# Optimization experiments

Hardware: AMD Instinct MI355X
Metric: run time of the kernel (lower is better)

## Reference

```python
import jax, jax.numpy as jnp
import numpy as np

B, S, D, H = 2, 1024, 1024, 16
DH = D // H            # dim per head = 64
MAX_REL = 32           # max relative positions
ROPE_BASE = 10000.0


def entmax15(X, axis=-1):
    """1.5-entmax with full sort (k=None path of the torch code)."""
    X = (X - jnp.max(X, axis=axis, keepdims=True)) / 2.0
    Xsrt = -jnp.sort(-X, axis=axis)                       # descending sort
    d = X.shape[axis]
    rho = jnp.arange(1, d + 1, dtype=X.dtype)             # broadcasts on last axis
    mean = jnp.cumsum(Xsrt, axis=axis) / rho
    mean_sq = jnp.cumsum(Xsrt * Xsrt, axis=axis) / rho
    ss = rho * (mean_sq - mean * mean)
    delta = (1.0 - ss) / rho
    tau = mean - jnp.sqrt(jnp.clip(delta, 0.0))
    support = jnp.sum(tau <= Xsrt, axis=axis, keepdims=True)
    tau_star = jnp.take_along_axis(tau, support - 1, axis=axis)
    Y = jnp.clip(X - tau_star, 0.0)
    return Y * Y


def _rope(x, cos, sin):
    # x: [B,S,H,DH]; cos/sin: [S, DH//2]; complex mult on (even,odd) pairs
    xe, xo = x[..., 0::2], x[..., 1::2]
    c = cos[None, :, None, :]
    s = sin[None, :, None, :]
    re = xe * c - xo * s
    im = xe * s + xo * c
    return jnp.stack([re, im], axis=-1).reshape(x.shape)


def setup_inputs() -> dict:
    key = jax.random.key(0)
    ks = jax.random.split(key, 10)
    sc = 0.02
    x = jax.random.normal(ks[0], (B, S, D), dtype=jnp.float32)
    w_q = jax.random.normal(ks[1], (D, D), dtype=jnp.float32) * sc
    w_k = jax.random.normal(ks[2], (D, D), dtype=jnp.float32) * sc
    w_v = jax.random.normal(ks[3], (D, D), dtype=jnp.float32) * sc
    w_o = jax.random.normal(ks[4], (D, D), dtype=jnp.float32) * sc
    b_q = jnp.zeros((D,), jnp.float32)
    b_k = jnp.zeros((D,), jnp.float32)
    b_v = jnp.zeros((D,), jnp.float32)
    b_o = jnp.zeros((D,), jnp.float32)
    rel_emb = jax.random.normal(ks[5], (2 * MAX_REL + 1, DH), dtype=jnp.float32) * sc
    inv_freq = 1.0 / (ROPE_BASE ** (np.arange(0, DH, 2, dtype=np.float32) / DH))
    ang = np.arange(S, dtype=np.float32)[:, None] * inv_freq[None, :]
    rope_cos = jnp.asarray(np.cos(ang), jnp.float32)
    rope_sin = jnp.asarray(np.sin(ang), jnp.float32)
    return {"x": x, "w_q": w_q, "b_q": b_q, "w_k": w_k, "b_k": b_k,
            "w_v": w_v, "b_v": b_v, "w_o": w_o, "b_o": b_o,
            "rel_emb": rel_emb, "rope_cos": rope_cos, "rope_sin": rope_sin}


def reference(x, w_q, b_q, w_k, b_k, w_v, b_v, w_o, b_o, rel_emb, rope_cos, rope_sin):
    # QKV projections -> [B,S,H,DH]
    q = (x @ w_q + b_q).reshape(B, S, H, DH)
    k = (x @ w_k + b_k).reshape(B, S, H, DH)
    v = (x @ w_v + b_v).reshape(B, S, H, DH).transpose(0, 2, 1, 3)  # [B,H,S,DH]
    # RoPE on q, k (applied in [B,S,H,DH] layout like the torch code)
    q = _rope(q, rope_cos, rope_sin).transpose(0, 2, 1, 3)  # [B,H,S,DH]
    k = _rope(k, rope_cos, rope_sin).transpose(0, 2, 1, 3)
    q = q / jnp.sqrt(jnp.asarray(DH, q.dtype))
    # content scores
    scores = jnp.einsum('bhqd,bhkd->bhqk', q, k)
    # relative position bias (Shaw et al.), shared embedding for keys & values
    r = jnp.arange(S)
    dist = jnp.clip(r[None, :] - r[:, None], -MAX_REL, MAX_REL) + MAX_REL  # [S,S]
    rel = rel_emb[dist]                                                   # [S,S,DH]
    scores = scores + jnp.einsum('bhqd,qkd->bhqk', q, rel)
    # sparse normalization
    attn = entmax15(scores, axis=-1)
    # context + relative-position values
    ctx = jnp.einsum('bhqk,bhkd->bhqd', attn, v) + jnp.einsum('bhqk,qkd->bhqd', attn, rel)
    out = ctx.transpose(0, 2, 1, 3).reshape(B, S, D) @ w_o + b_o
    return out
```

## Files before the change

kernel.cpp:

```cpp
#include <hip/hip_runtime.h>

typedef __attribute__((ext_vector_type(8))) short s8v;
typedef __attribute__((ext_vector_type(4))) short s4v;
typedef __attribute__((ext_vector_type(4))) float f4v;

__device__ __forceinline__ short f2bf(float f){
  union { float f; unsigned u; } v; v.f = f;
  unsigned r = v.u + 0x7fffu + ((v.u >> 16) & 1u);
  return (short)(r >> 16);
}
__device__ __forceinline__ float bf2f(short s){
  union { unsigned u; float f; } v; v.u = ((unsigned)(unsigned short)s) << 16; return v.f;
}

__global__ __launch_bounds__(256) void prep_k(const float* __restrict__ w_q, const float* __restrict__ w_k,
                                              const float* __restrict__ w_v, const float* __restrict__ w_o,
                                              const float* __restrict__ x, const float* __restrict__ rel,
                                              short* __restrict__ wqkvT, short* __restrict__ woT,
                                              short* __restrict__ xb, short* __restrict__ relb,
                                              short* __restrict__ relT){
  int z = blockIdx.z;
  if (z < 4){
    __shared__ float t[64][65];
    const float* in = (z==0) ? w_q : (z==1) ? w_k : (z==2) ? w_v : w_o;
    short* out = (z==3) ? woT : (wqkvT + ((size_t)z<<20));
    int c0 = blockIdx.x*64, r0 = blockIdx.y*64;
    int tx = threadIdx.x & 63, ty = threadIdx.x >> 6;
    #pragma unroll
    for (int i=0;i<16;i++){ int r = ty + i*4; t[r][tx] = in[(size_t)(r0+r)*1024 + c0+tx]; }
    __syncthreads();
    #pragma unroll
    for (int i=0;i<16;i++){ int cc = ty + i*4; out[(size_t)(c0+cc)*1024 + r0+tx] = f2bf(t[tx][cc]); }
    if (z==3 && blockIdx.x==0 && blockIdx.y==0){
      for (int e = threadIdx.x; e < 65*64; e += 256){
        int j = e >> 6, d = e & 63;
        short bv = f2bf(rel[e]);
        relb[e] = bv;
        relT[d*72 + j] = bv;
      }
    }
  } else {
    int bid = (z-4)*256 + blockIdx.y*16 + blockIdx.x;
    int i = bid*256 + threadIdx.x;
    #pragma unroll
    for (int p=0;p<4;p++){
      int idx = p*131072 + i;
      f4v v = ((const f4v*)x)[idx];
      s4v o; o[0]=f2bf(v[0]); o[1]=f2bf(v[1]); o[2]=f2bf(v[2]); o[3]=f2bf(v[3]);
      ((s4v*)xb)[idx] = o;
    }
  }
}

__device__ __forceinline__ void gemm128_core(const short* __restrict__ A, const short* __restrict__ Bt,
                                             int m0, int n0, short* As, short* Bs, f4v acc[4][4]){
  int tid = threadIdx.x;
  int lane = tid & 63, wave = tid >> 6;
  int wr = wave >> 1, wc = wave & 1, g = lane >> 4, c = lane & 15;
  int srow = tid >> 3, su = tid & 7;
  for (int k0 = 0; k0 < 1024; k0 += 64){
    #pragma unroll
    for (int p=0;p<4;p++){
      int r = srow + p*32;
      int u = su ^ (r & 7);
      *(s8v*)(&As[r*64 + u*8]) = *(const s8v*)(A + (size_t)(m0+r)*1024 + k0 + su*8);
      *(s8v*)(&Bs[r*64 + u*8]) = *(const s8v*)(Bt + (size_t)(n0+r)*1024 + k0 + su*8);
    }
    __syncthreads();
    #pragma unroll
    for (int ks=0;ks<2;ks++){
      s8v a[4], b[4];
      int pu = ((ks*4 + g) ^ (c & 7))*8;
      #pragma unroll
      for (int mi=0;mi<4;mi++) a[mi] = *(const s8v*)(&As[(wr*64 + mi*16 + c)*64 + pu]);
      #pragma unroll
      for (int ni=0;ni<4;ni++) b[ni] = *(const s8v*)(&Bs[(wc*64 + ni*16 + c)*64 + pu]);
      #pragma unroll
      for (int mi=0;mi<4;mi++)
        #pragma unroll
        for (int ni=0;ni<4;ni++)
          acc[mi][ni] = __builtin_amdgcn_mfma_f32_16x16x32_bf16(a[mi], b[ni], acc[mi][ni], 0,0,0);
    }
    __syncthreads();
  }
}

__global__ __launch_bounds__(256) void gemm_qkv_k(const short* __restrict__ A, const short* __restrict__ Bt,
                                                  const float* __restrict__ b_q, const float* __restrict__ b_k,
                                                  const float* __restrict__ b_v,
                                                  const float* __restrict__ cs, const float* __restrict__ sn,
                                                  short* __restrict__ Qb, short* __restrict__ Kb,
                                                  short* __restrict__ Vt){
  __shared__ __align__(16) char lbuf[33792];
  short* As = (short*)lbuf;
  short* Bs = (short*)(lbuf + 16384);
  short* st = (short*)lbuf;
  int flat = blockIdx.x;
  int swz = (flat & 7)*48 + (flat >> 3);
  int m0 = (swz / 24) * 128, n0 = (swz % 24) * 128;
  int lane = threadIdx.x & 63, wave = threadIdx.x >> 6;
  int wr = wave >> 1, wc = wave & 1, g = lane >> 4, c = lane & 15;
  f4v acc[4][4] = {};
  gemm128_core(A, Bt, m0, n0, As, Bs, acc);

  int sec = n0 >> 10;
  const float* bias = (sec==0) ? b_q : (sec==1) ? b_k : b_v;
  int b = m0 >> 10, s0 = m0 & 1023, hbase = (n0 & 1023) >> 6;
  #pragma unroll
  for (int mi=0;mi<4;mi++)
    #pragma unroll
    for (int ni=0;ni<4;ni++){
      int cl = wc*64 + ni*16 + c;
      int hcol = (n0 & 1023) + cl;
      float bi = bias[hcol];
      int d = hcol & 63, ifr = d >> 1;
      #pragma unroll
      for (int i=0;i<4;i++){
        int rl = wr*64 + mi*16 + g*4 + i;
        float v = acc[mi][ni][i] + bi;
        if (sec < 2){
          int s = s0 + rl;
          float co = cs[s*32 + ifr], si = sn[s*32 + ifr];
          float p = __shfl_xor(v, 1, 64);
          float o = (cl & 1) ? fmaf(p, si, v*co) : fmaf(v, co, -(p*si));
          if (sec == 0) o *= 0.125f;
          v = o;
        }
        st[rl*132 + cl] = f2bf(v);
      }
    }
  __syncthreads();
  if (sec < 2){
    short* dst = (sec==0) ? Qb : Kb;
    for (int e = threadIdx.x; e < 128*32; e += 256){
      int row = e >> 5, cl4 = (e & 31)*4;
      int h = hbase + (cl4 >> 6), d = cl4 & 63;
      s4v o = *(const s4v*)(&st[row*132 + cl4]);
      *(s4v*)(&dst[((size_t)(b*16+h)*1024 + s0 + row)*64 + d]) = o;
    }
  } else {
    for (int e = threadIdx.x; e < 128*32; e += 256){
      int cl = e >> 5, s4 = (e & 31)*4;
      int h = hbase + (cl >> 6), dl = cl & 63;
      s4v o;
      o[0] = st[(s4+0)*132 + cl]; o[1] = st[(s4+1)*132 + cl];
      o[2] = st[(s4+2)*132 + cl]; o[3] = st[(s4+3)*132 + cl];
      *(s4v*)(&Vt[(size_t)(b*16+h)*65536 + (size_t)dl*1024 + s0 + s4]) = o;
    }
  }
}

__global__ __launch_bounds__(256) void gemm_out_k(const short* __restrict__ A, const short* __restrict__ Bt,
                                                  const float* __restrict__ bias, float* __restrict__ C){
  __shared__ __align__(16) short As[128*64];
  __shared__ __align__(16) short Bs[128*64];
  int flat = blockIdx.x;
  int swz = (flat & 7)*16 + (flat >> 3);
  int n0 = (swz & 7)*128, m0 = (swz >> 3)*128;
  int lane = threadIdx.x & 63, wave = threadIdx.x >> 6;
  int wr = wave >> 1, wc = wave & 1, g = lane >> 4, c = lane & 15;
  f4v acc[4][4] = {};
  gemm128_core(A, Bt, m0, n0, As, Bs, acc);
  #pragma unroll
  for (int mi=0;mi<4;mi++)
    #pragma unroll
    for (int ni=0;ni<4;ni++){
      int col = n0 + wc*64 + ni*16 + c;
      float bi = bias[col];
      #pragma unroll
      for (int i=0;i<4;i++){
        int row = m0 + wr*64 + mi*16 + g*4 + i;
        C[(size_t)row*1024 + col] = acc[mi][ni][i] + bi;
      }
    }
}

#define ATPAD 1028
__global__ __launch_bounds__(256,4) void attn_fused_k(const short* __restrict__ Qb, const short* __restrict__ Kb,
                                                      const short* __restrict__ relb, const short* __restrict__ relT,
                                                      const short* __restrict__ Vt, short* __restrict__ ctxb){
  __shared__ __align__(16) short pb_b[16][66];
  __shared__ __align__(16) float wrow[16][68];
  __shared__ __align__(16) short attn_l[16][ATPAD];
  float2* red = (float2*)&pb_b[0][0];

  int lane = threadIdx.x & 63, wave = threadIdx.x >> 6;
  int g = lane >> 4, c = lane & 15;
  int flat = blockIdx.x;
  int swz = (flat & 7)*256 + (flat >> 3);
  int bh = swz >> 6, q0 = (swz & 63)*16;
  const short* Qh = Qb + (size_t)bh*65536;
  const short* Kh = Kb + (size_t)bh*65536;
  const short* Vh = Vt + (size_t)bh*65536;

  for (int e = threadIdx.x; e < 16*68; e += 256) ((float*)wrow)[e] = 0.f;

  s8v qa0 = *(const s8v*)(Qh + (q0+c)*64 + g*8);
  s8v qa1 = *(const s8v*)(Qh + (q0+c)*64 + 32 + g*8);

  {
    int ntile = (wave==3) ? 2 : 1;
    for (int t=0; t<ntile; t++){
      int jt = (t==0) ? wave : 4;
      int j = jt*16 + c;
      s8v rb0 = {}, rb1 = {};
      if (j < 65){
        rb0 = *(const s8v*)(relb + j*64 + g*8);
        rb1 = *(const s8v*)(relb + j*64 + 32 + g*8);
      }
      f4v pa = {};
      pa = __builtin_amdgcn_mfma_f32_16x16x32_bf16(qa0, rb0, pa, 0,0,0);
      pa = __builtin_amdgcn_mfma_f32_16x16x32_bf16(qa1, rb1, pa, 0,0,0);
      if (j < 65){
        #pragma unroll
        for (int i=0;i<4;i++) pb_b[g*4+i][j] = f2bf(pa[i]);
      }
    }
  }
  __syncthreads();

  int q = q0 + c;
  int kc0 = wave*256;
  f4v x[16];
  #pragma unroll
  for (int t=0;t<16;t++){
    f4v ini;
    #pragma unroll
    for (int i=0;i<4;i++){
      int k = kc0 + t*16 + g*4 + i;
      int jj = min(max(k - q, -32), 32) + 32;
      ini[i] = bf2f(pb_b[c][jj]);
    }
    const short* kp = Kh + (kc0 + t*16 + c)*64 + g*8;
    s8v ka0 = *(const s8v*)(kp);
    s8v ka1 = *(const s8v*)(kp + 32);
    ini = __builtin_amdgcn_mfma_f32_16x16x32_bf16(ka0, qa0, ini, 0,0,0);
    x[t] = __builtin_amdgcn_mfma_f32_16x16x32_bf16(ka1, qa1, ini, 0,0,0);
  }
  __syncthreads();

  float m0v = -1e30f, m1v = -1e30f, m2v = -1e30f, m3v = -1e30f;
  #pragma unroll
  for (int t=0;t<16;t++){
    m0v = fmaxf(m0v, x[t][0]); m1v = fmaxf(m1v, x[t][1]);
    m2v = fmaxf(m2v, x[t][2]); m3v = fmaxf(m3v, x[t][3]);
  }
  float mx = fmaxf(fmaxf(m0v,m1v), fmaxf(m2v,m3v));
  mx = fmaxf(mx, __shfl_xor(mx, 16, 64));
  mx = fmaxf(mx, __shfl_xor(mx, 32, 64));
  if (g == 0) red[wave*16 + c] = make_float2(mx, 0.f);
  __syncthreads();
  {
    float2 r0 = red[c], r1 = red[16+c], r2 = red[32+c], r3 = red[48+c];
    mx = fmaxf(fmaxf(r0.x, r1.x), fmaxf(r2.x, r3.x));
  }

  float theta = mx - 2.0f;
  for (int it=0; it<7; it++){
    float s1a=0.f,s1b=0.f,s1c=0.f,s1d=0.f, s2a=0.f,s2b=0.f,s2c=0.f,s2d=0.f;
    #pragma unroll
    for (int t=0;t<16;t++){
      float t0 = fmaxf(x[t][0]-theta, 0.f); s1a += t0; s2a = fmaf(t0,t0,s2a);
      float t1 = fmaxf(x[t][1]-theta, 0.f); s1b += t1; s2b = fmaf(t1,t1,s2b);
      float t2 = fmaxf(x[t][2]-theta, 0.f); s1c += t2; s2c = fmaf(t2,t2,s2c);
      float t3 = fmaxf(x[t][3]-theta, 0.f); s1d += t3; s2d = fmaf(t3,t3,s2d);
    }
    float S1 = (s1a+s1b)+(s1c+s1d), S2 = (s2a+s2b)+(s2c+s2d);
    S1 += __shfl_xor(S1, 16, 64); S2 += __shfl_xor(S2, 16, 64);
    S1 += __shfl_xor(S1, 32, 64); S2 += __shfl_xor(S2, 32, 64);
    int pp = (it+1)&1;
    if (g == 0) red[(pp*4 + wave)*16 + c] = make_float2(S1, S2);
    __syncthreads();
    float2 r0 = red[pp*64 + c], r1 = red[pp*64 + 16+c], r2 = red[pp*64 + 32+c], r3 = red[pp*64 + 48+c];
    S1 = (r0.x+r1.x)+(r2.x+r3.x);
    S2 = (r0.y+r1.y)+(r2.y+r3.y);
    theta += (S2 - 4.0f)/(2.0f*S1);
  }

  float w0p = 0.f, w64p = 0.f;
  #pragma unroll
  for (int t=0;t<16;t++){
    s4v pk;
    #pragma unroll
    for (int i=0;i<4;i++){
      int k = kc0 + t*16 + g*4 + i;
      float tt = fmaxf(x[t][i]-theta, 0.f)*0.5f;
      float a = tt*tt;
      pk[i] = f2bf(a);
      int raw = k - q;
      if (raw <= -32) w0p += a;
      else if (raw >= 32) w64p += a;
      else wrow[c][raw+32] = a;
    }
    *(s4v*)(&attn_l[c][kc0 + t*16 + g*4]) = pk;
  }
  w0p += __shfl_xor(w0p, 16, 64); w64p += __shfl_xor(w64p, 16, 64);
  w0p += __shfl_xor(w0p, 32, 64); w64p += __shfl_xor(w64p, 32, 64);
  if (g == 0) red[wave*16 + c] = make_float2(w0p, w64p);
  __syncthreads();
  if (wave == 0 && g == 0){
    float2 r0 = red[c], r1 = red[16+c], r2 = red[32+c], r3 = red[48+c];
    wrow[c][0]  = (r0.x+r1.x)+(r2.x+r3.x);
    wrow[c][64] = (r0.y+r1.y)+(r2.y+r3.y);
  }
  __syncthreads();

  f4v acc = {};
  #pragma unroll 8
  for (int kk=0; kk<32; kk++){
    s8v af = *(const s8v*)(&attn_l[c][kk*32 + g*8]);
    s8v bf = *(const s8v*)(Vh + (size_t)(wave*16+c)*1024 + kk*32 + g*8);
    acc = __builtin_amdgcn_mfma_f32_16x16x32_bf16(af, bf, acc, 0,0,0);
  }
  {
    const float* wp = &wrow[c][0];
    f4v a_ = *(const f4v*)(wp + g*8);
    f4v b_ = *(const f4v*)(wp + g*8 + 4);
    f4v c_ = *(const f4v*)(wp + 32 + g*8);
    f4v d_ = *(const f4v*)(wp + 32 + g*8 + 4);
    s8v wa0, wa1;
    wa0[0]=f2bf(a_[0]); wa0[1]=f2bf(a_[1]); wa0[2]=f2bf(a_[2]); wa0[3]=f2bf(a_[3]);
    wa0[4]=f2bf(b_[0]); wa0[5]=f2bf(b_[1]); wa0[6]=f2bf(b_[2]); wa0[7]=f2bf(b_[3]);
    wa1[0]=f2bf(c_[0]); wa1[1]=f2bf(c_[1]); wa1[2]=f2bf(c_[2]); wa1[3]=f2bf(c_[3]);
    wa1[4]=f2bf(d_[0]); wa1[5]=f2bf(d_[1]); wa1[6]=f2bf(d_[2]); wa1[7]=f2bf(d_[3]);
    s8v rb0 = *(const s8v*)(relT + (wave*16+c)*72 + g*8);
    s8v rb1 = *(const s8v*)(relT + (wave*16+c)*72 + 32 + g*8);
    acc = __builtin_amdgcn_mfma_f32_16x16x32_bf16(wa0, rb0, acc, 0,0,0);
    acc = __builtin_amdgcn_mfma_f32_16x16x32_bf16(wa1, rb1, acc, 0,0,0);
  }
  int b = bh >> 4, h = bh & 15, d = wave*16 + c;
  float rl64 = bf2f(relT[d*72 + 64]);
  #pragma unroll
  for (int i=0;i<4;i++){
    int r = g*4+i;
    float s = acc[i] + wrow[r][64]*rl64;
    ctxb[((size_t)(b*1024 + q0 + r))*1024 + h*64 + d] = f2bf(s);
  }
}

extern "C" void kernel_launch(void* const* d_in, const int* in_sizes, int n_in,
                              void* d_out, int out_size, void* d_ws, size_t ws_size,
                              hipStream_t stream) {
  (void)in_sizes; (void)n_in; (void)out_size; (void)ws_size;
  const float* x    = (const float*)d_in[0];
  const float* w_q  = (const float*)d_in[1];
  const float* b_q  = (const float*)d_in[2];
  const float* w_k  = (const float*)d_in[3];
  const float* b_k  = (const float*)d_in[4];
  const float* w_v  = (const float*)d_in[5];
  const float* b_v  = (const float*)d_in[6];
  const float* w_o  = (const float*)d_in[7];
  const float* b_o  = (const float*)d_in[8];
  const float* rel  = (const float*)d_in[9];
  const float* rcos = (const float*)d_in[10];
  const float* rsin = (const float*)d_in[11];
  float* out = (float*)d_out;

  char* w = (char*)d_ws;
  short* xb    = (short*)(w);
  short* wqkvT = (short*)(w + ((size_t)4<<20));
  short* woT   = (short*)(w + ((size_t)10<<20));
  short* Qb    = (short*)(w + ((size_t)12<<20));
  short* Kb    = (short*)(w + ((size_t)16<<20));
  short* Vt    = (short*)(w + ((size_t)20<<20));
  short* ctxb  = (short*)(w + ((size_t)24<<20));
  short* relb  = (short*)(w + ((size_t)28<<20));
  short* relT  = (short*)(w + ((size_t)28<<20) + 65536);

  prep_k<<<dim3(16,16,6), 256, 0, stream>>>(w_q, w_k, w_v, w_o, x, rel, wqkvT, woT, xb, relb, relT);
  gemm_qkv_k<<<384, 256, 0, stream>>>(xb, wqkvT, b_q, b_k, b_v, rcos, rsin, Qb, Kb, Vt);
  attn_fused_k<<<2048, 256, 0, stream>>>(Qb, Kb, relb, relT, Vt, ctxb);
  gemm_out_k<<<128, 256, 0, stream>>>(ctxb, woT, b_o, out);
}
```

Measured before the change: 138.4 us.

## Use direct global-to-LDS loads in GEMM and streamline entmax attention epilogue

The GEMM core now stages A and B tiles with global_load_lds 16-byte direct loads instead of register round-trips, and drops the XOR swizzle on the LDS layout. The attention kernel skips per-element relative-bias gathers and per-element bucket logic for tiles that lie entirely outside the relative window. It also vectorises the entmax threshold loops, uses hardware packed bf16 conversion, and raises wave priority around the PV MFMA loop. Removing the swizzle may bring back LDS bank conflicts on the fragment reads.

```diff
diff --git a/kernel.cpp b/kernel.cpp
--- a/kernel.cpp
+++ b/kernel.cpp
@@ -11,6 +11,10 @@
 }
 __device__ __forceinline__ float bf2f(short s){
   union { unsigned u; float f; } v; v.u = ((unsigned)(unsigned short)s) << 16; return v.f;
+}
+__device__ __forceinline__ void gload16(const void* g, void* l){
+  __builtin_amdgcn_global_load_lds((const __attribute__((address_space(1))) unsigned int*)g,
+                                   (__attribute__((address_space(3))) unsigned int*)l, 16, 0, 0);
 }
 
 __global__ __launch_bounds__(256) void prep_k(const float* __restrict__ w_q, const float* __restrict__ w_k,
@@ -57,20 +61,20 @@
   int tid = threadIdx.x;
   int lane = tid & 63, wave = tid >> 6;
   int wr = wave >> 1, wc = wave & 1, g = lane >> 4, c = lane & 15;
-  int srow = tid >> 3, su = tid & 7;
+  int lrow = lane >> 3, lcol = (lane & 7)*8;
   for (int k0 = 0; k0 < 1024; k0 += 64){
     #pragma unroll
     for (int p=0;p<4;p++){
-      int r = srow + p*32;
-      int u = su ^ (r & 7);
-      *(s8v*)(&As[r*64 + u*8]) = *(const s8v*)(A + (size_t)(m0+r)*1024 + k0 + su*8);
-      *(s8v*)(&Bs[r*64 + u*8]) = *(const s8v*)(Bt + (size_t)(n0+r)*1024 + k0 + su*8);
+      int r0 = wave*32 + p*8;
+      int row = r0 + lrow;
+      gload16(A  + (size_t)(m0+row)*1024 + k0 + lcol, &As[r0*64]);
+      gload16(Bt + (size_t)(n0+row)*1024 + k0 + lcol, &Bs[r0*64]);
     }
     __syncthreads();
     #pragma unroll
     for (int ks=0;ks<2;ks++){
       s8v a[4], b[4];
-      int pu = ((ks*4 + g) ^ (c & 7))*8;
+      int pu = ks*32 + g*8;
       #pragma unroll
       for (int mi=0;mi<4;mi++) a[mi] = *(const s8v*)(&As[(wr*64 + mi*16 + c)*64 + pu]);
       #pragma unroll
@@ -221,15 +225,23 @@
 
   int q = q0 + c;
   int kc0 = wave*256;
+  int Lb = q0 - 32 - kc0;
+  int Ub = q0 + 47 - kc0;
+  float pb0  = bf2f(pb_b[c][0]);
+  float pb64 = bf2f(pb_b[c][64]);
   f4v x[16];
   #pragma unroll
   for (int t=0;t<16;t++){
     f4v ini;
-    #pragma unroll
-    for (int i=0;i<4;i++){
-      int k = kc0 + t*16 + g*4 + i;
-      int jj = min(max(k - q, -32), 32) + 32;
-      ini[i] = bf2f(pb_b[c][jj]);
+    if (t*16+15 <= Lb){ ini[0]=pb0; ini[1]=pb0; ini[2]=pb0; ini[3]=pb0; }
+    else if (t*16 >= Ub){ ini[0]=pb64; ini[1]=pb64; ini[2]=pb64; ini[3]=pb64; }
+    else {
+      #pragma unroll
+      for (int i=0;i<4;i++){
+        int k = kc0 + t*16 + g*4 + i;
+        int jj = min(max(k - q, -32), 32) + 32;
+        ini[i] = bf2f(pb_b[c][jj]);
+      }
     }
     const short* kp = Kh + (kc0 + t*16 + c)*64 + g*8;
     s8v ka0 = *(const s8v*)(kp);
@@ -239,13 +251,13 @@
   }
   __syncthreads();
 
-  float m0v = -1e30f, m1v = -1e30f, m2v = -1e30f, m3v = -1e30f;
+  f4v m4 = x[0];
   #pragma unroll
-  for (int t=0;t<16;t++){
-    m0v = fmaxf(m0v, x[t][0]); m1v = fmaxf(m1v, x[t][1]);
-    m2v = fmaxf(m2v, x[t][2]); m3v = fmaxf(m3v, x[t][3]);
-  }
-  float mx = fmaxf(fmaxf(m0v,m1v), fmaxf(m2v,m3v));
+  for (int t=1;t<16;t++){
+    m4[0]=fmaxf(m4[0],x[t][0]); m4[1]=fmaxf(m4[1],x[t][1]);
+    m4[2]=fmaxf(m4[2],x[t][2]); m4[3]=fmaxf(m4[3],x[t][3]);
+  }
+  float mx = fmaxf(fmaxf(m4[0],m4[1]), fmaxf(m4[2],m4[3]));
   mx = fmaxf(mx, __shfl_xor(mx, 16, 64));
   mx = fmaxf(mx, __shfl_xor(mx, 32, 64));
   if (g == 0) red[wave*16 + c] = make_float2(mx, 0.f);
@@ -257,15 +269,18 @@
 
   float theta = mx - 2.0f;
   for (int it=0; it<7; it++){
-    float s1a=0.f,s1b=0.f,s1c=0.f,s1d=0.f, s2a=0.f,s2b=0.f,s2c=0.f,s2d=0.f;
+    f4v th4 = {theta, theta, theta, theta};
+    f4v s1v = {0.f,0.f,0.f,0.f}, s2v = {0.f,0.f,0.f,0.f};
     #pragma unroll
     for (int t=0;t<16;t++){
-      float t0 = fmaxf(x[t][0]-theta, 0.f); s1a += t0; s2a = fmaf(t0,t0,s2a);
-      float t1 = fmaxf(x[t][1]-theta, 0.f); s1b += t1; s2b = fmaf(t1,t1,s2b);
-      float t2 = fmaxf(x[t][2]-theta, 0.f); s1c += t2; s2c = fmaf(t2,t2,s2c);
-      float t3 = fmaxf(x[t][3]-theta, 0.f); s1d += t3; s2d = fmaf(t3,t3,s2d);
-    }
-    float S1 = (s1a+s1b)+(s1c+s1d), S2 = (s2a+s2b)+(s2c+s2d);
+      f4v d = x[t] - th4;
+      f4v tt;
+      tt[0]=fmaxf(d[0],0.f); tt[1]=fmaxf(d[1],0.f); tt[2]=fmaxf(d[2],0.f); tt[3]=fmaxf(d[3],0.f);
+      s1v += tt;
+      s2v += tt*tt;
+    }
+    float S1 = (s1v[0]+s1v[1])+(s1v[2]+s1v[3]);
+    float S2 = (s2v[0]+s2v[1])+(s2v[2]+s2v[3]);
     S1 += __shfl_xor(S1, 16, 64); S2 += __shfl_xor(S2, 16, 64);
     S1 += __shfl_xor(S1, 32, 64); S2 += __shfl_xor(S2, 32, 64);
     int pp = (it+1)&1;
@@ -278,21 +293,32 @@
   }
 
   float w0p = 0.f, w64p = 0.f;
-  #pragma unroll
-  for (int t=0;t<16;t++){
-    s4v pk;
-    #pragma unroll
-    for (int i=0;i<4;i++){
-      int k = kc0 + t*16 + g*4 + i;
-      float tt = fmaxf(x[t][i]-theta, 0.f)*0.5f;
-      float a = tt*tt;
-      pk[i] = f2bf(a);
-      int raw = k - q;
-      if (raw <= -32) w0p += a;
-      else if (raw >= 32) w64p += a;
-      else wrow[c][raw+32] = a;
-    }
-    *(s4v*)(&attn_l[c][kc0 + t*16 + g*4]) = pk;
+  {
+    f4v th4 = {theta, theta, theta, theta};
+    short* arow = &attn_l[c][kc0 + g*4];
+    #pragma unroll
+    for (int t=0;t<16;t++){
+      f4v d = x[t] - th4;
+      f4v tt;
+      tt[0]=fmaxf(d[0],0.f); tt[1]=fmaxf(d[1],0.f); tt[2]=fmaxf(d[2],0.f); tt[3]=fmaxf(d[3],0.f);
+      tt = tt*0.5f;
+      f4v a = tt*tt;
+      unsigned d0, d1;
+      asm("v_cvt_pk_bf16_f32 %0, %1, %2" : "=v"(d0) : "v"(a[0]), "v"(a[1]));
+      asm("v_cvt_pk_bf16_f32 %0, %1, %2" : "=v"(d1) : "v"(a[2]), "v"(a[3]));
+      *(uint2*)(arow + t*16) = make_uint2(d0, d1);
+      if (t*16+15 <= Lb)      w0p  += (a[0]+a[1])+(a[2]+a[3]);
+      else if (t*16 >= Ub)    w64p += (a[0]+a[1])+(a[2]+a[3]);
+      else {
+        #pragma unroll
+        for (int i=0;i<4;i++){
+          int raw = kc0 + t*16 + g*4 + i - q;
+          if (raw <= -32) w0p += a[i];
+          else if (raw >= 32) w64p += a[i];
+          else wrow[c][raw+32] = a[i];
+        }
+      }
+    }
   }
   w0p += __shfl_xor(w0p, 16, 64); w64p += __shfl_xor(w64p, 16, 64);
   w0p += __shfl_xor(w0p, 32, 64); w64p += __shfl_xor(w64p, 32, 64);
@@ -306,6 +332,7 @@
   __syncthreads();
 
   f4v acc = {};
+  __builtin_amdgcn_s_setprio(1);
   #pragma unroll 8
   for (int kk=0; kk<32; kk++){
     s8v af = *(const s8v*)(&attn_l[c][kk*32 + g*8]);
@@ -314,20 +341,25 @@
   }
   {
     const float* wp = &wrow[c][0];
-    f4v a_ = *(const f4v*)(wp + g*8);
-    f4v b_ = *(const f4v*)(wp + g*8 + 4);
-    f4v c_ = *(const f4v*)(wp + 32 + g*8);
-    f4v d_ = *(const f4v*)(wp + 32 + g*8 + 4);
-    s8v wa0, wa1;
-    wa0[0]=f2bf(a_[0]); wa0[1]=f2bf(a_[1]); wa0[2]=f2bf(a_[2]); wa0[3]=f2bf(a_[3]);
-    wa0[4]=f2bf(b_[0]); wa0[5]=f2bf(b_[1]); wa0[6]=f2bf(b_[2]); wa0[7]=f2bf(b_[3]);
-    wa1[0]=f2bf(c_[0]); wa1[1]=f2bf(c_[1]); wa1[2]=f2bf(c_[2]); wa1[3]=f2bf(c_[3]);
-    wa1[4]=f2bf(d_[0]); wa1[5]=f2bf(d_[1]); wa1[6]=f2bf(d_[2]); wa1[7]=f2bf(d_[3]);
+    f4v A0 = *(const f4v*)(wp + g*8);
+    f4v A1 = *(const f4v*)(wp + g*8 + 4);
+    f4v A2 = *(const f4v*)(wp + 32 + g*8);
+    f4v A3 = *(const f4v*)(wp + 32 + g*8 + 4);
+    union { unsigned u[4]; s8v v; } W0, W1;
+    asm("v_cvt_pk_bf16_f32 %0, %1, %2" : "=v"(W0.u[0]) : "v"(A0[0]), "v"(A0[1]));
+    asm("v_cvt_pk_bf16_f32 %0, %1, %2" : "=v"(W0.u[1]) : "v"(A0[2]), "v"(A0[3]));
+    asm("v_cvt_pk_bf16_f32 %0, %1, %2" : "=v"(W0.u[2]) : "v"(A1[0]), "v"(A1[1]));
+    asm("v_cvt_pk_bf16_f32 %0, %1, %2" : "=v"(W0.u[3]) : "v"(A1[2]), "v"(A1[3]));
+    asm("v_cvt_pk_bf16_f32 %0, %1, %2" : "=v"(W1.u[0]) : "v"(A2[0]), "v"(A2[1]));
+    asm("v_cvt_pk_bf16_f32 %0, %1, %2" : "=v"(W1.u[1]) : "v"(A2[2]), "v"(A2[3]));
+    asm("v_cvt_pk_bf16_f32 %0, %1, %2" : "=v"(W1.u[2]) : "v"(A3[0]), "v"(A3[1]));
+    asm("v_cvt_pk_bf16_f32 %0, %1, %2" : "=v"(W1.u[3]) : "v"(A3[2]), "v"(A3[3]));
     s8v rb0 = *(const s8v*)(relT + (wave*16+c)*72 + g*8);
     s8v rb1 = *(const s8v*)(relT + (wave*16+c)*72 + 32 + g*8);
-    acc = __builtin_amdgcn_mfma_f32_16x16x32_bf16(wa0, rb0, acc, 0,0,0);
-    acc = __builtin_amdgcn_mfma_f32_16x16x32_bf16(wa1, rb1, acc, 0,0,0);
-  }
+    acc = __builtin_amdgcn_mfma_f32_16x16x32_bf16(W0.v, rb0, acc, 0,0,0);
+    acc = __builtin_amdgcn_mfma_f32_16x16x32_bf16(W1.v, rb1, acc, 0,0,0);
+  }
+  __builtin_amdgcn_s_setprio(0);
   int b = bh >> 4, h = bh & 15, d = wave*16 + c;
   float rl64 = bf2f(relT[d*72 + 64]);
   #pragma unroll
```

After: 143.6 us. +3.7%, slower.
